# Performance work log

Measured on AMD Instinct MI355X. Metric: run time of the kernel, lower is better.

The kernel has to match this reference:

```python
import jax, jax.numpy as jnp
import numpy as np

N = 32768
NIN = 12
NC = 16
HID = 512
K = 8
B = 3.0
L = 8
D_HALF = NIN // 2                      # 6
DIN = D_HALF + NC                      # conditioner input
DOUT = (3 * K - 1) * (NIN - D_HALF)    # conditioner output
MIN_W = 1e-3
MIN_H = 1e-3
MIN_D = 1e-3
DERIV_CONST = float(np.log(np.exp(1.0 - MIN_D) - 1.0))  # softplus^{-1}(1-min_d)


def setup_inputs() -> dict:
    key = jax.random.key(0)
    ks = jax.random.split(key, 12)
    z = jax.random.normal(ks[0], (N, NIN), dtype=jnp.float32)
    c = jax.random.normal(ks[1], (N, NC), dtype=jnp.float32)

    def lin(k, fan_in, shape):
        bound = 1.0 / np.sqrt(fan_in)
        return jax.random.uniform(k, shape, jnp.float32, -bound, bound)

    W0 = lin(ks[2], DIN, (L, DIN, HID)); b0 = lin(ks[3], DIN, (L, HID))
    W1 = lin(ks[4], HID, (L, HID, HID)); b1 = lin(ks[5], HID, (L, HID))
    W2 = lin(ks[6], HID, (L, HID, HID)); b2 = lin(ks[7], HID, (L, HID))
    W3 = lin(ks[8], HID, (L, HID, DOUT)); b3 = lin(ks[9], HID, (L, DOUT))

    rng = np.random.default_rng(0)
    perms = jnp.asarray(np.stack([rng.permutation(NIN) for _ in range(L - 1)]),
                        dtype=jnp.int32)  # [L-1, NIN]
    return dict(z=z, c=c, W0=W0, b0=b0, W1=W1, b1=b1, W2=W2, b2=b2,
                W3=W3, b3=b3, perms=perms)


def _rqs(x, uw, uh, ud):
    """Unconstrained rational-quadratic spline (forward).
    x: [N, d2]; uw/uh: [N, d2, K]; ud: [N, d2, K+1] (already edge-padded)."""
    widths = jax.nn.softmax(uw, axis=-1)
    widths = MIN_W + (1.0 - MIN_W * K) * widths
    cw = jnp.cumsum(widths, axis=-1)
    cw = jnp.concatenate([jnp.zeros_like(cw[..., :1]), cw], axis=-1)
    cw = 2.0 * B * cw - B
    cw = cw.at[..., 0].set(-B).at[..., -1].set(B)
    w = cw[..., 1:] - cw[..., :-1]

    heights = jax.nn.softmax(uh, axis=-1)
    heights = MIN_H + (1.0 - MIN_H * K) * heights
    ch = jnp.cumsum(heights, axis=-1)
    ch = jnp.concatenate([jnp.zeros_like(ch[..., :1]), ch], axis=-1)
    ch = 2.0 * B * ch - B
    ch = ch.at[..., 0].set(-B).at[..., -1].set(B)
    h = ch[..., 1:] - ch[..., :-1]

    d = MIN_D + jax.nn.softplus(ud)  # [N, d2, K+1]

    xc = jnp.clip(x, -B, B)  # tails are handled by mask below
    # searchsorted: eps added only to the last knot for the search itself
    cw_search = cw.at[..., -1].add(1e-6)
    idx = jnp.clip(jnp.sum((xc[..., None] >= cw_search).astype(jnp.int32),
                           axis=-1) - 1, 0, K - 1)  # [N, d2]

    def g(a):
        return jnp.take_along_axis(a, idx[..., None], axis=-1)[..., 0]

    icw, iw = g(cw), g(w)
    ich, ih = g(ch), g(h)
    idelta = g(h / w)
    id0 = g(d)
    id1 = g(d[..., 1:])

    theta = (xc - icw) / iw
    t1m = theta * (1.0 - theta)
    num = ih * (idelta * theta**2 + id0 * t1m)
    den = idelta + (id0 + id1 - 2.0 * idelta) * t1m
    out = ich + num / den
    dnum = idelta**2 * (id1 * theta**2 + 2.0 * idelta * t1m
                        + id0 * (1.0 - theta)**2)
    lad = jnp.log(dnum) - 2.0 * jnp.log(den)

    inside = (x >= -B) & (x <= B)
    return jnp.where(inside, out, x), jnp.where(inside, lad, 0.0)


def _flow(z, c, W0, b0, W1, b1, W2, b2, W3, b3, perms):
    x = z
    total_ld = jnp.zeros(z.shape[0], dtype=z.dtype)
    for i in range(L):
        x1, x2 = x[:, :D_HALF], x[:, D_HALF:]
        inp = jnp.concatenate([x1, c], axis=-1)
        h0 = jax.nn.elu(inp @ W0[i] + b0[i])
        h1 = jax.nn.elu(h0 @ W1[i] + b1[i])
        h2 = jax.nn.elu(h1 @ W2[i] + b2[i])
        out = (h2 @ W3[i] + b3[i]).reshape(-1, NIN - D_HALF, 3 * K - 1)
        uw, uh, ud = out[..., :K], out[..., K:2 * K], out[..., 2 * K:]
        ud = jnp.pad(ud, ((0, 0), (0, 0), (1, 1)),
                     constant_values=DERIV_CONST)
        x2n, ld = _rqs(x2, uw, uh, ud)
        total_ld = total_ld + jnp.sum(ld, axis=-1)
        x = jnp.concatenate([x1, x2n], axis=-1)
        if i < L - 1:
            x = x[:, perms[i]]
    return x, total_ld


def reference(z, c, W0, b0, W1, b1, W2, b2, W3, b3, perms):
    return _flow(z, c, W0, b0, W1, b1, W2, b2, W3, b3, perms)
```

## Files before the change

kernel.cpp:

```cpp
#include <hip/hip_runtime.h>
#include <hip/hip_fp16.h>

#define NROWS   32768
#define MT      64
#define NTH     512
#define OS      148
#define BND     3.0f

typedef _Float16 half_t;
typedef __attribute__((ext_vector_type(8))) _Float16 f16x8;
typedef __attribute__((ext_vector_type(4))) _Float16 f16x4;
typedef __attribute__((ext_vector_type(4))) float    f32x4;


__global__ void pack_frag(const float* __restrict__ src, half_t* __restrict__ dst,
                          int K, int Nn, int NT, int KS) {
  int l = blockIdx.z;
  int frag = blockIdx.x * 4 + (threadIdx.x >> 6);
  int lane = threadIdx.x & 63;
  int NF = NT * KS;
  if (frag >= NF) return;
  int nt = frag / KS, ks = frag - nt * KS;
  int n = nt * 16 + (lane & 15);
  int kb = ks * 32 + (lane >> 4) * 8;
  f16x8 v;
#pragma unroll
  for (int e = 0; e < 8; e++) {
    int k = kb + e;
    v[e] = (k < K && n < Nn) ? (half_t)src[((size_t)l * K + k) * Nn + n] : (half_t)0.f;
  }
  *(f16x8*)(dst + ((size_t)l * NF + frag) * 512 + lane * 8) = v;
}

__device__ __forceinline__ float elu_f(float v) {
  return v > 0.f ? v : (__expf(v) - 1.f);
}

__device__ __forceinline__ void gemm_elu(
    const half_t* A, int KSA, int ksteps,
    const half_t* __restrict__ Wf, int KSW,
    const float* __restrict__ bias,
    half_t* dst,
    int w, int lane, int lm, int lk) {
  f16x8 a[2][4], b[4][2];
#pragma unroll
  for (int half = 0; half < 2; half++) {
    const int ntb = w * 4 + half * 2;
    f32x4 acc[4][2];
#pragma unroll
    for (int i = 0; i < 4; i++)
#pragma unroll
      for (int j = 0; j < 2; j++) acc[i][j] = (f32x4){0.f, 0.f, 0.f, 0.f};

    const bool prefilled = (ksteps == 16) && (half == 1);
    if (!prefilled) {
#pragma unroll
      for (int s = 0; s < 4; s++)
        if (s < ksteps) {
#pragma unroll
          for (int nt = 0; nt < 2; nt++)
            b[s][nt] = *(const f16x8*)(Wf + ((size_t)((ntb + nt) * KSW + s)) * 512 + lane * 8);
        }
#pragma unroll
      for (int s = 0; s < 2; s++)
        if (s < ksteps) {
#pragma unroll
          for (int mf = 0; mf < 4; mf++)
            a[s][mf] = *(const f16x8*)(A + ((size_t)(mf * KSA + s)) * 512 + lane * 8);
        }
    }
#pragma unroll
    for (int ks = 0; ks < ksteps; ks++) {
      const int sl = ks & 3, asx = ks & 1;
#pragma unroll
      for (int nt = 0; nt < 2; nt++)
#pragma unroll
        for (int mf = 0; mf < 4; mf++)
          acc[mf][nt] = __builtin_amdgcn_mfma_f32_16x16x32_f16(b[sl][nt], a[asx][mf], acc[mf][nt], 0, 0, 0);
      if (ks + 4 < ksteps) {
#pragma unroll
        for (int nt = 0; nt < 2; nt++)
          b[sl][nt] = *(const f16x8*)(Wf + ((size_t)((ntb + nt) * KSW + ks + 4)) * 512 + lane * 8);
      } else if (ksteps == 16 && half == 0) {
#pragma unroll
        for (int nt = 0; nt < 2; nt++)
          b[sl][nt] = *(const f16x8*)(Wf + ((size_t)((ntb + 2 + nt) * KSW + (ks - 12))) * 512 + lane * 8);
      }
      if (ks + 2 < ksteps) {
#pragma unroll
        for (int mf = 0; mf < 4; mf++)
          a[asx][mf] = *(const f16x8*)(A + ((size_t)(mf * KSA + ks + 2)) * 512 + lane * 8);
      } else if (ksteps == 16 && half == 0) {
#pragma unroll
        for (int mf = 0; mf < 4; mf++)
          a[asx][mf] = *(const f16x8*)(A + ((size_t)(mf * KSA + (ks - 14))) * 512 + lane * 8);
      }
    }
    {
      const int ksg = w * 2 + half;
#pragma unroll
      for (int nt = 0; nt < 2; nt++) {
        int n0 = w * 64 + half * 32 + nt * 16 + lk * 4;
        f32x4 bv = *(const f32x4*)(bias + n0);
        int lane_dst = (nt * 2 + (lk >> 1)) * 16 + lm;
#pragma unroll
        for (int mf = 0; mf < 4; mf++) {
          f16x4 pv;
#pragma unroll
          for (int r = 0; r < 4; r++) pv[r] = (half_t)elu_f(acc[mf][nt][r] + bv[r]);
          *(f16x4*)(dst + ((size_t)(mf * 16 + ksg)) * 512 + lane_dst * 8 + (lk & 1) * 4) = pv;
        }
      }
    }
  }
}

__device__ __forceinline__ void gemm_out(
    const half_t* A,
    const half_t* __restrict__ Wf,
    const float* __restrict__ bias,
    float* outb,
    int w, int lane, int lm, int lk) {
  f32x4 acc[4][2];
#pragma unroll
  for (int i = 0; i < 4; i++)
#pragma unroll
    for (int j = 0; j < 2; j++) acc[i][j] = (f32x4){0.f, 0.f, 0.f, 0.f};
  const bool has2 = (w == 0);

  f16x8 a[2][4], b[4][2];
#pragma unroll
  for (int s = 0; s < 4; s++) {
    b[s][0] = *(const f16x8*)(Wf + ((size_t)(w * 16 + s)) * 512 + lane * 8);
    if (has2) b[s][1] = *(const f16x8*)(Wf + ((size_t)(8 * 16 + s)) * 512 + lane * 8);
  }
#pragma unroll
  for (int s = 0; s < 2; s++) {
#pragma unroll
    for (int mf = 0; mf < 4; mf++)
      a[s][mf] = *(const f16x8*)(A + ((size_t)(mf * 16 + s)) * 512 + lane * 8);
  }
#pragma unroll
  for (int ks = 0; ks < 16; ks++) {
    const int sl = ks & 3, asx = ks & 1;
#pragma unroll
    for (int mf = 0; mf < 4; mf++)
      acc[mf][0] = __builtin_amdgcn_mfma_f32_16x16x32_f16(b[sl][0], a[asx][mf], acc[mf][0], 0, 0, 0);
    if (has2)
#pragma unroll
      for (int mf = 0; mf < 4; mf++)
        acc[mf][1] = __builtin_amdgcn_mfma_f32_16x16x32_f16(b[sl][1], a[asx][mf], acc[mf][1], 0, 0, 0);
    if (ks + 4 < 16) {
      b[sl][0] = *(const f16x8*)(Wf + ((size_t)(w * 16 + ks + 4)) * 512 + lane * 8);
      if (has2) b[sl][1] = *(const f16x8*)(Wf + ((size_t)(128 + ks + 4)) * 512 + lane * 8);
    }
    if (ks + 2 < 16) {
#pragma unroll
      for (int mf = 0; mf < 4; mf++)
        a[asx][mf] = *(const f16x8*)(A + ((size_t)(mf * 16 + ks + 2)) * 512 + lane * 8);
    }
  }
  {
    int n0 = w * 16 + lk * 4;
    f32x4 bv = *(const f32x4*)(bias + n0);
#pragma unroll
    for (int mf = 0; mf < 4; mf++) {
      f32x4 ov = acc[mf][0] + bv;
      *(f32x4*)(outb + (mf * 16 + lm) * OS + n0) = ov;
    }
  }
  if (has2) {
    int n0 = 128 + lk * 4;
    f32x4 bv;
#pragma unroll
    for (int r = 0; r < 4; r++) bv[r] = (n0 + r < 138) ? bias[n0 + r] : 0.f;
#pragma unroll
    for (int mf = 0; mf < 4; mf++) {
      f32x4 ov = acc[mf][1] + bv;
      *(f32x4*)(outb + (mf * 16 + lm) * OS + n0) = ov;
    }
  }
}

__global__ __launch_bounds__(NTH, 2) __attribute__((amdgpu_waves_per_eu(2, 2)))
void flow_kernel(const float* __restrict__ z, const float* __restrict__ c,
                 const float* __restrict__ b0, const float* __restrict__ b1,
                 const float* __restrict__ b2, const float* __restrict__ b3,
                 const int* __restrict__ perms,
                 const half_t* __restrict__ W0F, const half_t* __restrict__ W1F,
                 const half_t* __restrict__ W2F, const half_t* __restrict__ W3F,
                 float* __restrict__ out) {
  __shared__ half_t hbufA[4 * 16 * 512];
  __shared__ __align__(16) char smemB[4 * 16 * 512 * 2];
  __shared__ half_t inpb[4 * 512];
  __shared__ half_t cbuf[MT * 16];
  __shared__ float xbuf[MT][12];
  __shared__ float ldpart[MT][6];
  __shared__ float ldtot[MT];
  __shared__ int   permbuf[7][12];

  half_t* hbufB  = (half_t*)smemB;
  float*  outbuf = (float*)smemB;

  int tid = threadIdx.x;
  int w = tid >> 6, lane = tid & 63;
  int lm = lane & 15, lk = lane >> 4;
  int row0 = blockIdx.x * MT;

  for (int it = tid; it < MT * 12; it += NTH) xbuf[it / 12][it % 12] = z[(size_t)row0 * 12 + it];
  for (int it = tid; it < MT * 16; it += NTH) cbuf[it] = (half_t)c[(size_t)row0 * 16 + it];
  for (int it = tid; it < 84; it += NTH) permbuf[it / 12][it % 12] = perms[it];
  if (tid < MT) ldtot[tid] = 0.f;
  __syncthreads();

  for (int l = 0; l < 8; l++) {
    for (int it = tid; it < MT * 32; it += NTH) {
      int m = it >> 5, k = it & 31;
      half_t bv;
      if (k < 6)       bv = (half_t)xbuf[m][k];
      else if (k < 22) bv = cbuf[m * 16 + (k - 6)];
      else             bv = (half_t)0.f;
      inpb[(m >> 4) * 512 + ((k >> 3) * 16 + (m & 15)) * 8 + (k & 7)] = bv;
    }
    __syncthreads();
    gemm_elu(inpb, 1, 1,   W0F + (size_t)l * 32 * 512,     1,  b0 + l * 512, hbufA, w, lane, lm, lk);
    __syncthreads();
    gemm_elu(hbufA, 16, 16, W1F + (size_t)l * 512 * 512,  16,  b1 + l * 512, hbufB, w, lane, lm, lk);
    __syncthreads();
    gemm_elu(hbufB, 16, 16, W2F + (size_t)l * 512 * 512,  16,  b2 + l * 512, hbufA, w, lane, lm, lk);
    __syncthreads();
    gemm_out(hbufA, W3F + (size_t)l * 144 * 512, b3 + l * 138, outbuf, w, lane, lm, lk);
    __syncthreads();

    if (tid < MT * 6) {
      int m = tid / 6, j = tid % 6;
      const float* pr = outbuf + m * OS + j * 23;
      float uw[8], uh[8], dd[9];
#pragma unroll
      for (int i = 0; i < 8; i++) uw[i] = pr[i];
#pragma unroll
      for (int i = 0; i < 8; i++) uh[i] = pr[8 + i];
      dd[0] = 1.f; dd[8] = 1.f;
#pragma unroll
      for (int i = 0; i < 7; i++) {
        float u = pr[16 + i];
        float sp = (u > 15.f) ? u : __logf(1.f + __expf(u));
        dd[i + 1] = 0.001f + sp;
      }
      float mw = uw[0];
#pragma unroll
      for (int i = 1; i < 8; i++) mw = fmaxf(mw, uw[i]);
      float ew[8], sw = 0.f;
#pragma unroll
      for (int i = 0; i < 8; i++) { ew[i] = __expf(uw[i] - mw); sw += ew[i]; }
      float invw = 1.f / sw;
      float cw[9]; cw[0] = -BND;
      float a = 0.f;
#pragma unroll
      for (int i = 0; i < 8; i++) { a += 0.001f + 0.992f * ew[i] * invw; cw[i + 1] = 2.f * BND * a - BND; }
      cw[8] = BND;
      float mh = uh[0];
#pragma unroll
      for (int i = 1; i < 8; i++) mh = fmaxf(mh, uh[i]);
      float eh[8], sh = 0.f;
#pragma unroll
      for (int i = 0; i < 8; i++) { eh[i] = __expf(uh[i] - mh); sh += eh[i]; }
      float invh = 1.f / sh;
      float ch[9]; ch[0] = -BND;
      float ah = 0.f;
#pragma unroll
      for (int i = 0; i < 8; i++) { ah += 0.001f + 0.992f * eh[i] * invh; ch[i + 1] = 2.f * BND * ah - BND; }
      ch[8] = BND;

      float x2 = xbuf[m][6 + j];
      float xc = fminf(fmaxf(x2, -BND), BND);
      int cnt = 0;
#pragma unroll
      for (int i = 0; i < 9; i++) {
        float edge = (i == 8) ? (cw[8] + 1e-6f) : cw[i];
        cnt += (xc >= edge) ? 1 : 0;
      }
      int idx = cnt - 1; idx = idx < 0 ? 0 : (idx > 7 ? 7 : idx);
      float icw = cw[0], iw = cw[1] - cw[0], ich = ch[0], ih = ch[1] - ch[0], d0 = dd[0], d1 = dd[1];
#pragma unroll
      for (int i = 0; i < 8; i++) {
        if (idx == i) {
          icw = cw[i]; iw = cw[i + 1] - cw[i];
          ich = ch[i]; ih = ch[i + 1] - ch[i];
          d0 = dd[i]; d1 = dd[i + 1];
        }
      }
      float delta = ih / iw;
      float th  = (xc - icw) / iw;
      float t1m = th * (1.f - th);
      float num = ih * (delta * th * th + d0 * t1m);
      float den = delta + (d0 + d1 - 2.f * delta) * t1m;
      float outv = ich + num / den;
      float dnum = delta * delta * (d1 * th * th + 2.f * delta * t1m + d0 * (1.f - th) * (1.f - th));
      float lad = __logf(dnum) - 2.f * __logf(den);
      bool inside = (x2 >= -BND) && (x2 <= BND);
      xbuf[m][6 + j] = inside ? outv : x2;
      ldpart[m][j]   = inside ? lad : 0.f;
    }
    __syncthreads();
    if (tid < MT) {
      float s = ldtot[tid];
#pragma unroll
      for (int j = 0; j < 6; j++) s += ldpart[tid][j];
      ldtot[tid] = s;
    }
    if (l < 7) {
      float v0 = xbuf[tid / 12][permbuf[l][tid % 12]];
      float v1 = 0.f;
      int it1 = tid + NTH;
      if (it1 < MT * 12) v1 = xbuf[it1 / 12][permbuf[l][it1 % 12]];
      __syncthreads();
      xbuf[tid / 12][tid % 12] = v0;
      if (it1 < MT * 12) xbuf[it1 / 12][it1 % 12] = v1;
    }
    __syncthreads();
  }

  for (int it = tid; it < MT * 12; it += NTH) out[(size_t)row0 * 12 + it] = xbuf[it / 12][it % 12];
  if (tid < MT) out[(size_t)NROWS * 12 + row0 + tid] = ldtot[tid];
}

extern "C" void kernel_launch(void* const* d_in, const int* in_sizes, int n_in,
                              void* d_out, int out_size, void* d_ws, size_t ws_size,
                              hipStream_t stream) {
  const float* z  = (const float*)d_in[0];
  const float* c  = (const float*)d_in[1];
  const float* W0 = (const float*)d_in[2];
  const float* b0 = (const float*)d_in[3];
  const float* W1 = (const float*)d_in[4];
  const float* b1 = (const float*)d_in[5];
  const float* W2 = (const float*)d_in[6];
  const float* b2 = (const float*)d_in[7];
  const float* W3 = (const float*)d_in[8];
  const float* b3 = (const float*)d_in[9];
  const int* perms = (const int*)d_in[10];

  unsigned short* wsu = (unsigned short*)d_ws;
  half_t* W0F = (half_t*)(wsu + 0);
  half_t* W1F = (half_t*)(wsu + 131072);
  half_t* W2F = (half_t*)(wsu + 2228224);
  half_t* W3F = (half_t*)(wsu + 4325376);

  pack_frag<<<dim3(8,   1, 8), dim3(256), 0, stream>>>(W0, W0F, 22,  512, 32, 1);
  pack_frag<<<dim3(128, 1, 8), dim3(256), 0, stream>>>(W1, W1F, 512, 512, 32, 16);
  pack_frag<<<dim3(128, 1, 8), dim3(256), 0, stream>>>(W2, W2F, 512, 512, 32, 16);
  pack_frag<<<dim3(36,  1, 8), dim3(256), 0, stream>>>(W3, W3F, 512, 138, 9,  16);

  flow_kernel<<<dim3(NROWS / MT), dim3(NTH), 0, stream>>>(
      z, c, b0, b1, b2, b3, perms, W0F, W1F, W2F, W3F, (float*)d_out);
}
```

Baseline: 472.3 us.

## Double block threads to 16 waves and split GEMM N-tiles per wave

```diff
diff --git a/kernel.cpp b/kernel.cpp
--- a/kernel.cpp
+++ b/kernel.cpp
@@ -3,7 +3,7 @@
 
 #define NROWS   32768
 #define MT      64
-#define NTH     512
+#define NTH     1024
 #define OS      148
 #define BND     3.0f
 
@@ -43,73 +43,60 @@
     half_t* dst,
     int w, int lane, int lm, int lk) {
   f16x8 a[2][4], b[4][2];
-#pragma unroll
-  for (int half = 0; half < 2; half++) {
-    const int ntb = w * 4 + half * 2;
-    f32x4 acc[4][2];
-#pragma unroll
-    for (int i = 0; i < 4; i++)
-#pragma unroll
-      for (int j = 0; j < 2; j++) acc[i][j] = (f32x4){0.f, 0.f, 0.f, 0.f};
-
-    const bool prefilled = (ksteps == 16) && (half == 1);
-    if (!prefilled) {
-#pragma unroll
-      for (int s = 0; s < 4; s++)
-        if (s < ksteps) {
-#pragma unroll
-          for (int nt = 0; nt < 2; nt++)
-            b[s][nt] = *(const f16x8*)(Wf + ((size_t)((ntb + nt) * KSW + s)) * 512 + lane * 8);
-        }
-#pragma unroll
-      for (int s = 0; s < 2; s++)
-        if (s < ksteps) {
-#pragma unroll
-          for (int mf = 0; mf < 4; mf++)
-            a[s][mf] = *(const f16x8*)(A + ((size_t)(mf * KSA + s)) * 512 + lane * 8);
-        }
-    }
-#pragma unroll
-    for (int ks = 0; ks < ksteps; ks++) {
-      const int sl = ks & 3, asx = ks & 1;
+  const int ntb = w * 2;
+  f32x4 acc[4][2];
+#pragma unroll
+  for (int i = 0; i < 4; i++)
+#pragma unroll
+    for (int j = 0; j < 2; j++) acc[i][j] = (f32x4){0.f, 0.f, 0.f, 0.f};
+
+#pragma unroll
+  for (int s = 0; s < 4; s++)
+    if (s < ksteps) {
 #pragma unroll
       for (int nt = 0; nt < 2; nt++)
-#pragma unroll
-        for (int mf = 0; mf < 4; mf++)
-          acc[mf][nt] = __builtin_amdgcn_mfma_f32_16x16x32_f16(b[sl][nt], a[asx][mf], acc[mf][nt], 0, 0, 0);
-      if (ks + 4 < ksteps) {
-#pragma unroll
-        for (int nt = 0; nt < 2; nt++)
-          b[sl][nt] = *(const f16x8*)(Wf + ((size_t)((ntb + nt) * KSW + ks + 4)) * 512 + lane * 8);
-      } else if (ksteps == 16 && half == 0) {
-#pragma unroll
-        for (int nt = 0; nt < 2; nt++)
-          b[sl][nt] = *(const f16x8*)(Wf + ((size_t)((ntb + 2 + nt) * KSW + (ks - 12))) * 512 + lane * 8);
-      }
-      if (ks + 2 < ksteps) {
-#pragma unroll
-        for (int mf = 0; mf < 4; mf++)
-          a[asx][mf] = *(const f16x8*)(A + ((size_t)(mf * KSA + ks + 2)) * 512 + lane * 8);
-      } else if (ksteps == 16 && half == 0) {
-#pragma unroll
-        for (int mf = 0; mf < 4; mf++)
-          a[asx][mf] = *(const f16x8*)(A + ((size_t)(mf * KSA + (ks - 14))) * 512 + lane * 8);
-      }
-    }
-    {
-      const int ksg = w * 2 + half;
-#pragma unroll
-      for (int nt = 0; nt < 2; nt++) {
-        int n0 = w * 64 + half * 32 + nt * 16 + lk * 4;
-        f32x4 bv = *(const f32x4*)(bias + n0);
-        int lane_dst = (nt * 2 + (lk >> 1)) * 16 + lm;
-#pragma unroll
-        for (int mf = 0; mf < 4; mf++) {
-          f16x4 pv;
-#pragma unroll
-          for (int r = 0; r < 4; r++) pv[r] = (half_t)elu_f(acc[mf][nt][r] + bv[r]);
-          *(f16x4*)(dst + ((size_t)(mf * 16 + ksg)) * 512 + lane_dst * 8 + (lk & 1) * 4) = pv;
-        }
+        b[s][nt] = *(const f16x8*)(Wf + ((size_t)((ntb + nt) * KSW + s)) * 512 + lane * 8);
+    }
+#pragma unroll
+  for (int s = 0; s < 2; s++)
+    if (s < ksteps) {
+#pragma unroll
+      for (int mf = 0; mf < 4; mf++)
+        a[s][mf] = *(const f16x8*)(A + ((size_t)(mf * KSA + s)) * 512 + lane * 8);
+    }
+
+#pragma unroll
+  for (int ks = 0; ks < ksteps; ks++) {
+    const int sl = ks & 3, asx = ks & 1;
+#pragma unroll
+    for (int nt = 0; nt < 2; nt++)
+#pragma unroll
+      for (int mf = 0; mf < 4; mf++)
+        acc[mf][nt] = __builtin_amdgcn_mfma_f32_16x16x32_f16(b[sl][nt], a[asx][mf], acc[mf][nt], 0, 0, 0);
+    if (ks + 4 < ksteps) {
+#pragma unroll
+      for (int nt = 0; nt < 2; nt++)
+        b[sl][nt] = *(const f16x8*)(Wf + ((size_t)((ntb + nt) * KSW + ks + 4)) * 512 + lane * 8);
+    }
+    if (ks + 2 < ksteps) {
+#pragma unroll
+      for (int mf = 0; mf < 4; mf++)
+        a[asx][mf] = *(const f16x8*)(A + ((size_t)(mf * KSA + ks + 2)) * 512 + lane * 8);
+    }
+  }
+  {
+    const int ksg = w;
+#pragma unroll
+    for (int nt = 0; nt < 2; nt++) {
+      int n0 = w * 32 + nt * 16 + lk * 4;
+      f32x4 bv = *(const f32x4*)(bias + n0);
+      int lane_dst = (nt * 2 + (lk >> 1)) * 16 + lm;
+#pragma unroll
+      for (int mf = 0; mf < 4; mf++) {
+        f16x4 pv;
+#pragma unroll
+        for (int r = 0; r < 4; r++) pv[r] = (half_t)elu_f(acc[mf][nt][r] + bv[r]);
+        *(f16x4*)(dst + ((size_t)(mf * 16 + ksg)) * 512 + lane_dst * 8 + (lk & 1) * 4) = pv;
       }
     }
   }
@@ -121,19 +108,15 @@
     const float* __restrict__ bias,
     float* outb,
     int w, int lane, int lm, int lk) {
-  f32x4 acc[4][2];
-#pragma unroll
-  for (int i = 0; i < 4; i++)
-#pragma unroll
-    for (int j = 0; j < 2; j++) acc[i][j] = (f32x4){0.f, 0.f, 0.f, 0.f};
-  const bool has2 = (w == 0);
-
-  f16x8 a[2][4], b[4][2];
-#pragma unroll
-  for (int s = 0; s < 4; s++) {
-    b[s][0] = *(const f16x8*)(Wf + ((size_t)(w * 16 + s)) * 512 + lane * 8);
-    if (has2) b[s][1] = *(const f16x8*)(Wf + ((size_t)(8 * 16 + s)) * 512 + lane * 8);
-  }
+  if (w >= 9) return;
+  f32x4 acc[4];
+#pragma unroll
+  for (int i = 0; i < 4; i++) acc[i] = (f32x4){0.f, 0.f, 0.f, 0.f};
+
+  f16x8 a[2][4], b[4];
+#pragma unroll
+  for (int s = 0; s < 4; s++)
+    b[s] = *(const f16x8*)(Wf + ((size_t)(w * 16 + s)) * 512 + lane * 8);
 #pragma unroll
   for (int s = 0; s < 2; s++) {
 #pragma unroll
@@ -145,15 +128,9 @@
     const int sl = ks & 3, asx = ks & 1;
 #pragma unroll
     for (int mf = 0; mf < 4; mf++)
-      acc[mf][0] = __builtin_amdgcn_mfma_f32_16x16x32_f16(b[sl][0], a[asx][mf], acc[mf][0], 0, 0, 0);
-    if (has2)
-#pragma unroll
-      for (int mf = 0; mf < 4; mf++)
-        acc[mf][1] = __builtin_amdgcn_mfma_f32_16x16x32_f16(b[sl][1], a[asx][mf], acc[mf][1], 0, 0, 0);
-    if (ks + 4 < 16) {
-      b[sl][0] = *(const f16x8*)(Wf + ((size_t)(w * 16 + ks + 4)) * 512 + lane * 8);
-      if (has2) b[sl][1] = *(const f16x8*)(Wf + ((size_t)(128 + ks + 4)) * 512 + lane * 8);
-    }
+      acc[mf] = __builtin_amdgcn_mfma_f32_16x16x32_f16(b[sl], a[asx][mf], acc[mf], 0, 0, 0);
+    if (ks + 4 < 16)
+      b[sl] = *(const f16x8*)(Wf + ((size_t)(w * 16 + ks + 4)) * 512 + lane * 8);
     if (ks + 2 < 16) {
 #pragma unroll
       for (int mf = 0; mf < 4; mf++)
@@ -162,27 +139,22 @@
   }
   {
     int n0 = w * 16 + lk * 4;
-    f32x4 bv = *(const f32x4*)(bias + n0);
+    f32x4 bv;
+    if (w < 8) {
+      bv = *(const f32x4*)(bias + n0);
+    } else {
+#pragma unroll
+      for (int r = 0; r < 4; r++) bv[r] = (n0 + r < 138) ? bias[n0 + r] : 0.f;
+    }
 #pragma unroll
     for (int mf = 0; mf < 4; mf++) {
-      f32x4 ov = acc[mf][0] + bv;
+      f32x4 ov = acc[mf] + bv;
       *(f32x4*)(outb + (mf * 16 + lm) * OS + n0) = ov;
     }
   }
-  if (has2) {
-    int n0 = 128 + lk * 4;
-    f32x4 bv;
-#pragma unroll
-    for (int r = 0; r < 4; r++) bv[r] = (n0 + r < 138) ? bias[n0 + r] : 0.f;
-#pragma unroll
-    for (int mf = 0; mf < 4; mf++) {
-      f32x4 ov = acc[mf][1] + bv;
-      *(f32x4*)(outb + (mf * 16 + lm) * OS + n0) = ov;
-    }
-  }
-}
-
-__global__ __launch_bounds__(NTH, 2) __attribute__((amdgpu_waves_per_eu(2, 2)))
+}
+
+__global__ __launch_bounds__(NTH, 4) __attribute__((amdgpu_waves_per_eu(4, 4)))
 void flow_kernel(const float* __restrict__ z, const float* __restrict__ c,
                  const float* __restrict__ b0, const float* __restrict__ b1,
                  const float* __restrict__ b2, const float* __restrict__ b3,
@@ -310,13 +282,10 @@
       ldtot[tid] = s;
     }
     if (l < 7) {
-      float v0 = xbuf[tid / 12][permbuf[l][tid % 12]];
-      float v1 = 0.f;
-      int it1 = tid + NTH;
-      if (it1 < MT * 12) v1 = xbuf[it1 / 12][permbuf[l][it1 % 12]];
+      float v0 = 0.f;
+      if (tid < MT * 12) v0 = xbuf[tid / 12][permbuf[l][tid % 12]];
       __syncthreads();
-      xbuf[tid / 12][tid % 12] = v0;
-      if (it1 < MT * 12) xbuf[it1 / 12][it1 % 12] = v1;
+      if (tid < MT * 12) xbuf[tid / 12][tid % 12] = v0;
     }
     __syncthreads();
   }
```

After: 589.1 us. +24.7%, slower.
